# Performance work log

Measured on AMD Instinct MI355X. Metric: run time of the kernel, lower is better.

The kernel has to match this reference:

```python
import jax, jax.numpy as jnp
import numpy as np

T, B, V, E, H = 128, 32, 32000, 512, 1024
PAD = 0

def setup_inputs() -> dict:
    key = jax.random.key(0)
    ks = jax.random.split(key, 10)
    indices = jax.random.randint(ks[0], (T, B), 0, V)
    emb = jax.random.normal(ks[1], (V, E), jnp.float32) * 0.02
    s = 1.0 / np.sqrt(H).astype(np.float32)
    W_ih = jax.random.normal(ks[2], (4 * H, E), jnp.float32) * s
    W_hh = jax.random.normal(ks[3], (4 * H, H), jnp.float32) * s
    b_ih = jax.random.normal(ks[4], (4 * H,), jnp.float32) * 0.01
    b_hh = jax.random.normal(ks[5], (4 * H,), jnp.float32) * 0.01
    W_out = jax.random.normal(ks[6], (V, H), jnp.float32) * s
    b_out = jnp.zeros((V,), jnp.float32)
    h0 = jax.random.uniform(ks[7], (B, H), jnp.float32, -0.1, 0.1)
    c0 = jax.random.uniform(ks[8], (B, H), jnp.float32, -0.1, 0.1)
    return dict(indices=indices, emb=emb, W_ih=W_ih, W_hh=W_hh,
                b_ih=b_ih, b_hh=b_hh, W_out=W_out, b_out=b_out, h0=h0, c0=c0)

def reference(indices, emb, W_ih, W_hh, b_ih, b_hh, W_out, b_out, h0, c0):
    # embed + relu for all timesteps at once (dropout_rate=0.0 -> identity)
    x_all = jax.nn.relu(emb[indices[:-1]])   # [T-1, B, E]
    targets = indices[1:]                    # [T-1, B]

    def step(carry, inp):
        h, c, loss = carry
        x, tgt = inp
        # torch LSTM gate order: i, f, g, o
        gates = x @ W_ih.T + b_ih + h @ W_hh.T + b_hh   # [B, 4H]
        i, f, g, o = jnp.split(gates, 4, axis=-1)
        c = jax.nn.sigmoid(f) * c + jax.nn.sigmoid(i) * jnp.tanh(g)
        h = jax.nn.sigmoid(o) * jnp.tanh(c)
        logp = jax.nn.log_softmax(h @ W_out.T + b_out, axis=-1)  # [B, V]
        nll = -jnp.take_along_axis(logp, tgt[:, None], axis=-1)[:, 0]
        # NLLLoss(reduction='sum', ignore_index=PAD)
        loss = loss + jnp.sum(jnp.where(tgt != PAD, nll, 0.0))
        return (h, c, loss), None

    (_, _, loss), _ = jax.lax.scan(step, (h0, c0, jnp.float32(0.0)), (x_all, targets))
    return loss
```

## Files before the change

kernel.cpp:

```cpp
#include <hip/hip_runtime.h>
#include <hip/hip_bf16.h>
#include <hip/hip_cooperative_groups.h>
#include <math.h>

namespace cg = cooperative_groups;

typedef __bf16 bf16_t;
typedef bf16_t bf16x8 __attribute__((ext_vector_type(8)));
typedef float f32x4 __attribute__((ext_vector_type(4)));
typedef unsigned u32x2 __attribute__((ext_vector_type(2)));

#define T_SEQ 128
#define NB 32
#define NV 32000
#define NE 512
#define NH 1024
#define G4 4096
#define MROWS 4064
#define MPAD 4096

#define NBLK 256

__device__ __forceinline__ void g2lds16(const bf16_t* g, bf16_t* l) {
  __builtin_amdgcn_global_load_lds((const __attribute__((address_space(1))) void*)g,
                                   (__attribute__((address_space(3))) void*)l, 16, 0, 0);
}

__device__ __forceinline__ unsigned short bf16bits(float x) {
  bf16_t b = (bf16_t)x;
  return __builtin_bit_cast(unsigned short, b);
}

__global__ void k_prep(const int* __restrict__ idx, const float* __restrict__ emb,
                       const float* __restrict__ W_ih, const float* __restrict__ W_hh,
                       const float* __restrict__ b_ih, const float* __restrict__ b_hh,
                       const float* __restrict__ W_out, const float* __restrict__ h0,
                       bf16_t* __restrict__ W_ih_bf, bf16_t* __restrict__ W_hh_bf,
                       bf16_t* __restrict__ W_out_bf, bf16_t* __restrict__ x_bf,
                       bf16_t* __restrict__ h_all, bf16_t* __restrict__ h0_bf,
                       float* __restrict__ bc, float* __restrict__ rowS,
                       int* __restrict__ tgt, unsigned* __restrict__ bar) {
  const long nW_ih = 4096L * 512;
  const long nW_hh = 4096L * 1024;
  const long nW_out = 32000L * 1024;
  const long nX = 4096L * 512;
  const long nH0 = 32L * 1024;
  const long nHpad = 32L * 1024;
  const long NTOTAL = nW_ih + nW_hh + nW_out + nX + nH0 + nHpad + 3 * 4096L + 1024;
  long stride = (long)gridDim.x * blockDim.x;
  for (long i = (long)blockIdx.x * blockDim.x + threadIdx.x; i < NTOTAL; i += stride) {
    long j = i;
    if (j < nW_ih) { W_ih_bf[j] = (bf16_t)W_ih[j]; continue; }
    j -= nW_ih;
    if (j < nW_hh) { W_hh_bf[j] = (bf16_t)W_hh[j]; continue; }
    j -= nW_hh;
    if (j < nW_out) { W_out_bf[j] = (bf16_t)W_out[j]; continue; }
    j -= nW_out;
    if (j < nX) {
      long m = j >> 9; int e = (int)(j & 511);
      float x = 0.f;
      if (m < MROWS) { x = emb[(long)idx[m] * NE + e]; x = x > 0.f ? x : 0.f; }
      x_bf[j] = (bf16_t)x; continue;
    }
    j -= nX;
    if (j < nH0) { h0_bf[j] = (bf16_t)h0[j]; continue; }
    j -= nH0;
    if (j < nHpad) { h_all[4161536L + j] = (bf16_t)0.f; continue; }
    j -= nHpad;
    if (j < 4096) { bc[j] = b_ih[j] + b_hh[j]; continue; }
    j -= 4096;
    if (j < 4096) { rowS[j] = 0.f; continue; }
    j -= 4096;
    if (j < 4096) { tgt[j] = (j < MROWS) ? idx[j + NB] : 0; continue; }
    j -= 4096;
    { bar[j] = 0u; continue; }
  }
}

__global__ __launch_bounds__(256) void k_gemm1(const bf16_t* __restrict__ A,
                                               const bf16_t* __restrict__ B,
                                               const float* __restrict__ bc,
                                               bf16_t* __restrict__ C) {
  const int K = 512;
  int tid = threadIdx.x, wid = tid >> 6, lane = tid & 63;
  int wm = wid & 1, wn = wid >> 1;
  int quad = lane >> 4, l15 = lane & 15;
  int mBase = blockIdx.x * 64, nBase = blockIdx.y * 128;

  const bf16x8* pa0 = (const bf16x8*)(A + (long)(mBase + wm * 32 + l15) * K + quad * 8);
  const bf16x8* pa1 = (const bf16x8*)(A + (long)(mBase + wm * 32 + 16 + l15) * K + quad * 8);
  const bf16x8* pb[4];
#pragma unroll
  for (int j = 0; j < 4; ++j)
    pb[j] = (const bf16x8*)(B + (long)(nBase + wn * 64 + j * 16 + l15) * K + quad * 8);

  f32x4 acc[2][4];
#pragma unroll
  for (int mi = 0; mi < 2; ++mi)
#pragma unroll
    for (int ni = 0; ni < 4; ++ni) acc[mi][ni] = (f32x4){0.f, 0.f, 0.f, 0.f};

  for (int kk = 0; kk < K / 32; ++kk) {
    bf16x8 a0 = pa0[kk * 4], a1 = pa1[kk * 4];
    bf16x8 b0 = pb[0][kk * 4], b1 = pb[1][kk * 4], b2 = pb[2][kk * 4], b3 = pb[3][kk * 4];
    acc[0][0] = __builtin_amdgcn_mfma_f32_16x16x32_bf16(a0, b0, acc[0][0], 0, 0, 0);
    acc[0][1] = __builtin_amdgcn_mfma_f32_16x16x32_bf16(a0, b1, acc[0][1], 0, 0, 0);
    acc[0][2] = __builtin_amdgcn_mfma_f32_16x16x32_bf16(a0, b2, acc[0][2], 0, 0, 0);
    acc[0][3] = __builtin_amdgcn_mfma_f32_16x16x32_bf16(a0, b3, acc[0][3], 0, 0, 0);
    acc[1][0] = __builtin_amdgcn_mfma_f32_16x16x32_bf16(a1, b0, acc[1][0], 0, 0, 0);
    acc[1][1] = __builtin_amdgcn_mfma_f32_16x16x32_bf16(a1, b1, acc[1][1], 0, 0, 0);
    acc[1][2] = __builtin_amdgcn_mfma_f32_16x16x32_bf16(a1, b2, acc[1][2], 0, 0, 0);
    acc[1][3] = __builtin_amdgcn_mfma_f32_16x16x32_bf16(a1, b3, acc[1][3], 0, 0, 0);
  }
#pragma unroll
  for (int ni = 0; ni < 4; ++ni) {
    int col = nBase + wn * 64 + ni * 16 + l15;
    float bcv = bc[col];
#pragma unroll
    for (int mi = 0; mi < 2; ++mi)
#pragma unroll
      for (int r = 0; r < 4; ++r) {
        int row = mBase + wm * 32 + mi * 16 + quad * 4 + r;
        C[(long)row * G4 + col] = (bf16_t)(acc[mi][ni][r] + bcv);
      }
  }
}

__global__ __launch_bounds__(512) void k_rec8(const bf16_t* __restrict__ gates_x,
                                              const bf16_t* __restrict__ W_hh_bf,
                                              const bf16_t* __restrict__ h0_bf,
                                              bf16_t* __restrict__ h_all,
                                              const float* __restrict__ c0,
                                              unsigned* __restrict__ bar) {
  __shared__ __align__(16) float red[32 * 68];

  int bid = blockIdx.x;
  int mi = bid & 1;
  int hb = bid >> 1;
  int gbase = hb * 8;
  int tid = threadIdx.x, wid = tid >> 6, lane = tid & 63;
  int cg = wid & 1, kh = wid >> 1;
  int quad = lane >> 4, l15 = lane & 15;

  unsigned* genp = bar + mi * 512 + 288;
  unsigned* flagp = bar + mi * 512 + 320 + hb;
  const unsigned* fp2 = bar + mi * 512 + 320 + (lane << 1);
  bool isagg = (bid < 2) && (wid == 7);

  int wrow = (cg ? 2048 : 0) + ((l15 & 8) ? 1024 : 0) + gbase + (l15 & 7);
  const bf16x8* pw = (const bf16x8*)(W_hh_bf + (long)wrow * NH + kh * 256 + quad * 8);
  bf16x8 wfrag[8];
#pragma unroll
  for (int kk = 0; kk < 8; ++kk) wfrag[kk] = pw[kk * 4];

  int pb = tid >> 2, pu2 = (tid & 3) * 2;
  int u0 = gbase + pu2;
  int bglob = mi * 16 + pb;
  float cst0 = 0.f, cst1 = 0.f;
  if (tid < 64) {
    cst0 = c0[(long)bglob * NH + u0];
    cst1 = c0[(long)bglob * NH + u0 + 1];
  }
  unsigned* h32 = (unsigned*)h_all;

  for (int t = 0; t < T_SEQ - 1; ++t) {
    unsigned gxi2 = 0, gxf2 = 0, gxg2 = 0, gxo2 = 0;
    if (tid < 64) {
      const unsigned* gp = (const unsigned*)(gates_x + (long)(t * NB + bglob) * G4);
      int q = u0 >> 1;
      gxi2 = gp[q]; gxf2 = gp[512 + q]; gxg2 = gp[1024 + q]; gxo2 = gp[1536 + q];
    }

    if (t > 0) {
      if (isagg) {
        unsigned need = (unsigned)t;
        while (1) {
          u32x2 fv;
          asm volatile("global_load_dwordx2 %0, %1, off sc0 sc1\n\t"
                       "s_waitcnt vmcnt(0)"
                       : "=&v"(fv) : "v"(fp2) : "memory");
          if (__all((fv.x >= need) & (fv.y >= need))) break;
          __builtin_amdgcn_s_sleep(1);
        }
        if (lane == 0)
          __hip_atomic_store(genp, (unsigned)t, __ATOMIC_RELAXED,
                             __HIP_MEMORY_SCOPE_AGENT);
      }
      if (tid == 0) {
        unsigned need = (unsigned)t;
        while (__hip_atomic_load(genp, __ATOMIC_RELAXED,
                                 __HIP_MEMORY_SCOPE_AGENT) < need)
          __builtin_amdgcn_s_sleep(1);
      }
    }
    __syncthreads();
    asm volatile("" ::: "memory");

    const bf16_t* hp = (t == 0) ? h0_bf : (h_all + (long)(t - 1) * NB * NH);
    const bf16x8* pa = (const bf16x8*)(hp + (long)(mi * 16 + l15) * NH + kh * 256 + quad * 8);
    f32x4 acc = (f32x4){0.f, 0.f, 0.f, 0.f};
#pragma unroll
    for (int kk = 0; kk < 8; ++kk) {
      bf16x8 a = pa[kk * 4];
      acc = __builtin_amdgcn_mfma_f32_16x16x32_bf16(a, wfrag[kk], acc, 0, 0, 0);
    }
#pragma unroll
    for (int r = 0; r < 4; ++r) {
      int row = (cg << 4) + (quad << 2) + r;
      red[row * 68 + (l15 << 2) + kh] = acc[r];
    }
    __syncthreads();

    if (tid < 64) {
      const float* rc = red;
      float hv[2];
#pragma unroll
      for (int d = 0; d < 2; ++d) {
        int q = pu2 + d;
        float4 vi = *(const float4*)(rc + pb * 68 + (q << 2));
        float4 vf = *(const float4*)(rc + pb * 68 + ((8 + q) << 2));
        float4 vg = *(const float4*)(rc + (16 + pb) * 68 + (q << 2));
        float4 vo = *(const float4*)(rc + (16 + pb) * 68 + ((8 + q) << 2));
        unsigned bi = d ? (gxi2 & 0xffff0000u) : (gxi2 << 16);
        unsigned bff = d ? (gxf2 & 0xffff0000u) : (gxf2 << 16);
        unsigned bg = d ? (gxg2 & 0xffff0000u) : (gxg2 << 16);
        unsigned bo = d ? (gxo2 & 0xffff0000u) : (gxo2 << 16);
        float iv = vi.x + vi.y + vi.z + vi.w + __builtin_bit_cast(float, bi);
        float fv = vf.x + vf.y + vf.z + vf.w + __builtin_bit_cast(float, bff);
        float gv = vg.x + vg.y + vg.z + vg.w + __builtin_bit_cast(float, bg);
        float ov = vo.x + vo.y + vo.z + vo.w + __builtin_bit_cast(float, bo);
        float si = 1.f / (1.f + __expf(-iv));
        float sf = 1.f / (1.f + __expf(-fv));
        float so = 1.f / (1.f + __expf(-ov));
        float tg = 1.f - 2.f / (__expf(2.f * gv) + 1.f);
        float& cs = d ? cst1 : cst0;
        cs = sf * cs + si * tg;
        float th = 1.f - 2.f / (__expf(2.f * cs) + 1.f);
        hv[d] = so * th;
      }
      unsigned pack = (unsigned)bf16bits(hv[0]) | ((unsigned)bf16bits(hv[1]) << 16);
      __hip_atomic_store(&h32[(long)(t * NB + bglob) * 512 + (u0 >> 1)], pack,
                         __ATOMIC_RELAXED, __HIP_MEMORY_SCOPE_AGENT);
      if (t < T_SEQ - 2) {
        asm volatile("" ::: "memory");
        if (tid == 0) {
          __builtin_amdgcn_s_waitcnt(0x0f70);
          asm volatile("" ::: "memory");
          __hip_atomic_store(flagp, (unsigned)(t + 1), __ATOMIC_RELAXED,
                             __HIP_MEMORY_SCOPE_AGENT);
        }
      }
    }
  }
}

__global__ __launch_bounds__(256) void k_gemm2(const bf16_t* __restrict__ A,
                                               const bf16_t* __restrict__ B,
                                               const float* __restrict__ b_out,
                                               float* __restrict__ rowS) {
  __shared__ bf16_t As[128 * 32];
  __shared__ bf16_t Bs[128 * 32];
  const int K = 1024;
  int tid = threadIdx.x, wid = tid >> 6, lane = tid & 63;
  int wm = wid & 1, wn = wid >> 1;
  int quad = lane >> 4, l15 = lane & 15;
  int mBase = blockIdx.x * 128, nBase = blockIdx.y * 128;

  int rc = lane >> 2, seg = lane & 3;
  int cA0 = 2 * wid, cA1 = 2 * wid + 1;
  const bf16_t* gA0 = A + (size_t)(mBase + cA0 * 16 + rc) * K + seg * 8;
  const bf16_t* gA1 = A + (size_t)(mBase + cA1 * 16 + rc) * K + seg * 8;
  const bf16_t* gB0 = B + (size_t)(nBase + cA0 * 16 + rc) * K + seg * 8;
  const bf16_t* gB1 = B + (size_t)(nBase + cA1 * 16 + rc) * K + seg * 8;
  bf16_t* lA0 = As + cA0 * 512;
  bf16_t* lA1 = As + cA1 * 512;
  bf16_t* lB0 = Bs + cA0 * 512;
  bf16_t* lB1 = Bs + cA1 * 512;

  const bf16x8* pa[4];
  const bf16x8* pbf[4];
#pragma unroll
  for (int i = 0; i < 4; ++i) {
    pa[i] = (const bf16x8*)(As + (wm * 64 + i * 16 + l15) * 32 + quad * 8);
    pbf[i] = (const bf16x8*)(Bs + (wn * 64 + i * 16 + l15) * 32 + quad * 8);
  }

  f32x4 acc[4][4];
#pragma unroll
  for (int i = 0; i < 4; ++i)
#pragma unroll
    for (int j = 0; j < 4; ++j) acc[i][j] = (f32x4){0.f, 0.f, 0.f, 0.f};

  for (int kt = 0; kt < K / 32; ++kt) {
    g2lds16(gA0 + kt * 32, lA0);
    g2lds16(gA1 + kt * 32, lA1);
    g2lds16(gB0 + kt * 32, lB0);
    g2lds16(gB1 + kt * 32, lB1);
    __syncthreads();

    bf16x8 af[4], bf[4];
#pragma unroll
    for (int i = 0; i < 4; ++i) { af[i] = *pa[i]; bf[i] = *pbf[i]; }
#pragma unroll
    for (int i = 0; i < 4; ++i)
#pragma unroll
      for (int j = 0; j < 4; ++j)
        acc[i][j] = __builtin_amdgcn_mfma_f32_16x16x32_bf16(af[i], bf[j], acc[i][j], 0, 0, 0);
    __syncthreads();
  }

#pragma unroll
  for (int i = 0; i < 4; ++i) {
    float rs[4] = {0.f, 0.f, 0.f, 0.f};
#pragma unroll
    for (int j = 0; j < 4; ++j) {
      int col = nBase + wn * 64 + j * 16 + l15;
      float bb = b_out[col];
#pragma unroll
      for (int r = 0; r < 4; ++r) rs[r] += __expf(acc[i][j][r] + bb);
    }
#pragma unroll
    for (int r = 0; r < 4; ++r) {
#pragma unroll
      for (int s = 1; s < 16; s <<= 1) rs[r] += __shfl_xor(rs[r], s);
      if (l15 == 0) {
        int row = mBase + wm * 64 + i * 16 + quad * 4 + r;
        if (row < MROWS) atomicAdd(&rowS[row], rs[r]);
      }
    }
  }
}

__global__ __launch_bounds__(256) void k_tgt(const bf16_t* __restrict__ h_all,
                                             const bf16_t* __restrict__ W_out_bf,
                                             const float* __restrict__ b_out,
                                             const int* __restrict__ tgt,
                                             float* __restrict__ tgt_logit) {
  int gw = (int)((blockIdx.x * blockDim.x + threadIdx.x) >> 6);
  int lane = threadIdx.x & 63;
  if (gw >= MROWS) return;
  int v = tgt[gw];
  const bf16x8* ph = (const bf16x8*)(h_all + (long)gw * NH + lane * 16);
  const bf16x8* pw = (const bf16x8*)(W_out_bf + (long)v * NH + lane * 16);
  float acc = 0.f;
#pragma unroll
  for (int j = 0; j < 2; ++j) {
    bf16x8 h8 = ph[j], w8 = pw[j];
#pragma unroll
    for (int q = 0; q < 8; ++q) acc += (float)h8[q] * (float)w8[q];
  }
#pragma unroll
  for (int s = 1; s < 64; s <<= 1) acc += __shfl_xor(acc, s);
  if (lane == 0) tgt_logit[gw] = acc + b_out[v];
}

__global__ __launch_bounds__(256) void k_loss(const float* __restrict__ rowS,
                                              const float* __restrict__ tl,
                                              const int* __restrict__ tgt,
                                              float* __restrict__ out) {
  __shared__ float sm[256];
  float s = 0.f;
  for (int i = threadIdx.x; i < MROWS; i += 256)
    if (tgt[i] != 0) s += logf(rowS[i]) - tl[i];
  sm[threadIdx.x] = s;
  __syncthreads();
  for (int off = 128; off > 0; off >>= 1) {
    if (threadIdx.x < off) sm[threadIdx.x] += sm[threadIdx.x + off];
    __syncthreads();
  }
  if (threadIdx.x == 0) out[0] = sm[0];
}

extern "C" void kernel_launch(void* const* d_in, const int* in_sizes, int n_in,
                              void* d_out, int out_size, void* d_ws, size_t ws_size,
                              hipStream_t stream) {
  const int* idx = (const int*)d_in[0];
  const float* emb = (const float*)d_in[1];
  const float* W_ih = (const float*)d_in[2];
  const float* W_hh = (const float*)d_in[3];
  const float* b_ih = (const float*)d_in[4];
  const float* b_hh = (const float*)d_in[5];
  const float* W_out = (const float*)d_in[6];
  const float* b_out = (const float*)d_in[7];
  const float* h0 = (const float*)d_in[8];
  const float* c0 = (const float*)d_in[9];

  char* ws = (char*)d_ws;
  bf16_t* W_ih_bf = (bf16_t*)ws;            ws += 4096L * 512 * 2;
  bf16_t* W_hh_bf = (bf16_t*)ws;            ws += 4096L * 1024 * 2;
  bf16_t* W_out_bf = (bf16_t*)ws;           ws += 32000L * 1024 * 2;
  bf16_t* x_bf = (bf16_t*)ws;               ws += 4096L * 512 * 2;
  bf16_t* gates_x = (bf16_t*)ws;            ws += 4096L * 4096 * 2;
  bf16_t* h_all = (bf16_t*)ws;              ws += 4096L * 1024 * 2;
  bf16_t* h0_bf = (bf16_t*)ws;              ws += 32L * 1024 * 2;
  float* bc = (float*)ws;                   ws += 4096L * 4;
  float* rowS = (float*)ws;                 ws += 4096L * 4;
  float* tgt_logit = (float*)ws;            ws += 4096L * 4;
  int* tgt = (int*)ws;                      ws += 4096L * 4;
  unsigned* bar = (unsigned*)ws;            ws += 1024L * 4;

  k_prep<<<4096, 256, 0, stream>>>(idx, emb, W_ih, W_hh, b_ih, b_hh, W_out, h0,
                                   W_ih_bf, W_hh_bf, W_out_bf, x_bf, h_all, h0_bf,
                                   bc, rowS, tgt, bar);

  k_gemm1<<<dim3(64, 32), 256, 0, stream>>>(x_bf, W_ih_bf, bc, gates_x);

  {
    void* args[] = {(void*)&gates_x, (void*)&W_hh_bf, (void*)&h0_bf, (void*)&h_all,
                    (void*)&c0, (void*)&bar};
    hipLaunchCooperativeKernel((void*)k_rec8, dim3(NBLK), dim3(512), args, 0, stream);
  }

  k_gemm2<<<dim3(32, 250), 256, 0, stream>>>(h_all, W_out_bf, b_out, rowS);

  k_tgt<<<1016, 256, 0, stream>>>(h_all, W_out_bf, b_out, tgt, tgt_logit);

  k_loss<<<1, 256, 0, stream>>>(rowS, tgt_logit, tgt, (float*)d_out);
}
```

Measured before the change: 1.332 ms.

## Use sentinel-filled hidden state to replace store-wait before flag in recurrence

The prep kernel now converts weights and embeddings four elements at a time with vectorized loads and stores, and fills the h_all buffer with a 0xFFFFFFFF sentinel. The recurrent kernel drops the s_waitcnt that made the flag store wait for the h stores to complete. Instead, readers check each loaded h fragment for the sentinel and re-poll with cache-bypassing loads until real data arrives. This takes the store-drain latency off the per-step critical path, at the cost of extra compare work and possible spin reloads, and it relies on no valid bf16 pair ever matching the sentinel pattern.

```diff
diff --git a/kernel.cpp b/kernel.cpp
--- a/kernel.cpp
+++ b/kernel.cpp
@@ -9,6 +9,7 @@
 typedef bf16_t bf16x8 __attribute__((ext_vector_type(8)));
 typedef float f32x4 __attribute__((ext_vector_type(4)));
 typedef unsigned u32x2 __attribute__((ext_vector_type(2)));
+typedef unsigned u32x4 __attribute__((ext_vector_type(4)));
 
 #define T_SEQ 128
 #define NB 32
@@ -20,6 +21,7 @@
 #define MPAD 4096
 
 #define NBLK 256
+#define SENT 0xFFFFFFFFu
 
 __device__ __forceinline__ void g2lds16(const bf16_t* g, bf16_t* l) {
   __builtin_amdgcn_global_load_lds((const __attribute__((address_space(1))) void*)g,
@@ -29,6 +31,15 @@
 __device__ __forceinline__ unsigned short bf16bits(float x) {
   bf16_t b = (bf16_t)x;
   return __builtin_bit_cast(unsigned short, b);
+}
+
+__device__ __forceinline__ void cvt4(const float* __restrict__ s,
+                                     bf16_t* __restrict__ d, long j) {
+  float4 v = *(const float4*)(s + j * 4);
+  uint2 o;
+  o.x = (unsigned)bf16bits(v.x) | ((unsigned)bf16bits(v.y) << 16);
+  o.y = (unsigned)bf16bits(v.z) | ((unsigned)bf16bits(v.w) << 16);
+  *(uint2*)(d + j * 4) = o;
 }
 
 __global__ void k_prep(const int* __restrict__ idx, const float* __restrict__ emb,
@@ -40,33 +51,47 @@
                        bf16_t* __restrict__ h_all, bf16_t* __restrict__ h0_bf,
                        float* __restrict__ bc, float* __restrict__ rowS,
                        int* __restrict__ tgt, unsigned* __restrict__ bar) {
-  const long nW_ih = 4096L * 512;
-  const long nW_hh = 4096L * 1024;
-  const long nW_out = 32000L * 1024;
-  const long nX = 4096L * 512;
-  const long nH0 = 32L * 1024;
-  const long nHpad = 32L * 1024;
-  const long NTOTAL = nW_ih + nW_hh + nW_out + nX + nH0 + nHpad + 3 * 4096L + 1024;
+  const long n4_Wih = 4096L * 512 / 4;
+  const long n4_Whh = 4096L * 1024 / 4;
+  const long n4_Wout = 32000L * 1024 / 4;
+  const long n4_X = 4096L * 512 / 4;
+  const long n4_H0 = 32L * 1024 / 4;
+  const long n4_Hall = 4096L * 1024 / 8;
+  const long nSentinel = 4064L * 128;
+  const long nScal = 3 * 4096L + 1024;
+  const long NTOT = n4_Wih + n4_Whh + n4_Wout + n4_X + n4_H0 + n4_Hall + nScal;
   long stride = (long)gridDim.x * blockDim.x;
-  for (long i = (long)blockIdx.x * blockDim.x + threadIdx.x; i < NTOTAL; i += stride) {
+  for (long i = (long)blockIdx.x * blockDim.x + threadIdx.x; i < NTOT; i += stride) {
     long j = i;
-    if (j < nW_ih) { W_ih_bf[j] = (bf16_t)W_ih[j]; continue; }
-    j -= nW_ih;
-    if (j < nW_hh) { W_hh_bf[j] = (bf16_t)W_hh[j]; continue; }
-    j -= nW_hh;
-    if (j < nW_out) { W_out_bf[j] = (bf16_t)W_out[j]; continue; }
-    j -= nW_out;
-    if (j < nX) {
-      long m = j >> 9; int e = (int)(j & 511);
-      float x = 0.f;
-      if (m < MROWS) { x = emb[(long)idx[m] * NE + e]; x = x > 0.f ? x : 0.f; }
-      x_bf[j] = (bf16_t)x; continue;
-    }
-    j -= nX;
-    if (j < nH0) { h0_bf[j] = (bf16_t)h0[j]; continue; }
-    j -= nH0;
-    if (j < nHpad) { h_all[4161536L + j] = (bf16_t)0.f; continue; }
-    j -= nHpad;
+    if (j < n4_Wih) { cvt4(W_ih, W_ih_bf, j); continue; }
+    j -= n4_Wih;
+    if (j < n4_Whh) { cvt4(W_hh, W_hh_bf, j); continue; }
+    j -= n4_Whh;
+    if (j < n4_Wout) { cvt4(W_out, W_out_bf, j); continue; }
+    j -= n4_Wout;
+    if (j < n4_X) {
+      long m = j >> 7; int e4 = (int)(j & 127);
+      uint2 o; o.x = 0u; o.y = 0u;
+      if (m < MROWS) {
+        float4 v = *(const float4*)(emb + (long)idx[m] * NE + e4 * 4);
+        v.x = fmaxf(v.x, 0.f); v.y = fmaxf(v.y, 0.f);
+        v.z = fmaxf(v.z, 0.f); v.w = fmaxf(v.w, 0.f);
+        o.x = (unsigned)bf16bits(v.x) | ((unsigned)bf16bits(v.y) << 16);
+        o.y = (unsigned)bf16bits(v.z) | ((unsigned)bf16bits(v.w) << 16);
+      }
+      *(uint2*)(x_bf + m * 512 + e4 * 4) = o;
+      continue;
+    }
+    j -= n4_X;
+    if (j < n4_H0) { cvt4(h0, h0_bf, j); continue; }
+    j -= n4_H0;
+    if (j < n4_Hall) {
+      unsigned v = (j < nSentinel) ? SENT : 0u;
+      uint4 s; s.x = v; s.y = v; s.z = v; s.w = v;
+      ((uint4*)h_all)[j] = s;
+      continue;
+    }
+    j -= n4_Hall;
     if (j < 4096) { bc[j] = b_ih[j] + b_hh[j]; continue; }
     j -= 4096;
     if (j < 4096) { rowS[j] = 0.f; continue; }
@@ -126,7 +151,7 @@
   }
 }
 
-__global__ __launch_bounds__(512) void k_rec8(const bf16_t* __restrict__ gates_x,
+__global__ __launch_bounds__(512) void k_rec9(const bf16_t* __restrict__ gates_x,
                                               const bf16_t* __restrict__ W_hh_bf,
                                               const bf16_t* __restrict__ h0_bf,
                                               bf16_t* __restrict__ h_all,
@@ -196,14 +221,47 @@
     __syncthreads();
     asm volatile("" ::: "memory");
 
-    const bf16_t* hp = (t == 0) ? h0_bf : (h_all + (long)(t - 1) * NB * NH);
-    const bf16x8* pa = (const bf16x8*)(hp + (long)(mi * 16 + l15) * NH + kh * 256 + quad * 8);
+    bf16x8 hfr[8];
+    if (t == 0) {
+      const bf16x8* pa0 =
+          (const bf16x8*)(h0_bf + (long)(mi * 16 + l15) * NH + kh * 256 + quad * 8);
+#pragma unroll
+      for (int kk = 0; kk < 8; ++kk) hfr[kk] = pa0[kk * 4];
+    } else {
+      const bf16_t* hb8 = h_all + (long)(t - 1) * NB * NH +
+                          (long)(mi * 16 + l15) * NH + kh * 256 + quad * 8;
+      const bf16x8* pa = (const bf16x8*)hb8;
+#pragma unroll
+      for (int kk = 0; kk < 8; ++kk) hfr[kk] = pa[kk * 4];
+      unsigned bad = 0;
+#pragma unroll
+      for (int kk = 0; kk < 8; ++kk) {
+        u32x4 w = __builtin_bit_cast(u32x4, hfr[kk]);
+        bad |= (unsigned)(w.x == SENT) | (unsigned)(w.y == SENT) |
+               (unsigned)(w.z == SENT) | (unsigned)(w.w == SENT);
+      }
+      while (!__all(bad == 0)) {
+        __builtin_amdgcn_s_sleep(1);
+        u32x4 hw[8];
+#pragma unroll
+        for (int kk = 0; kk < 8; ++kk)
+          asm volatile("global_load_dwordx4 %0, %1, off sc0 sc1"
+                       : "=&v"(hw[kk]) : "v"(hb8 + kk * 32) : "memory");
+        asm volatile("s_waitcnt vmcnt(0)" ::: "memory");
+        bad = 0;
+#pragma unroll
+        for (int kk = 0; kk < 8; ++kk) {
+          bad |= (unsigned)(hw[kk].x == SENT) | (unsigned)(hw[kk].y == SENT) |
+                 (unsigned)(hw[kk].z == SENT) | (unsigned)(hw[kk].w == SENT);
+          hfr[kk] = __builtin_bit_cast(bf16x8, hw[kk]);
+        }
+      }
+    }
+
     f32x4 acc = (f32x4){0.f, 0.f, 0.f, 0.f};
 #pragma unroll
-    for (int kk = 0; kk < 8; ++kk) {
-      bf16x8 a = pa[kk * 4];
-      acc = __builtin_amdgcn_mfma_f32_16x16x32_bf16(a, wfrag[kk], acc, 0, 0, 0);
-    }
+    for (int kk = 0; kk < 8; ++kk)
+      acc = __builtin_amdgcn_mfma_f32_16x16x32_bf16(hfr[kk], wfrag[kk], acc, 0, 0, 0);
 #pragma unroll
     for (int r = 0; r < 4; ++r) {
       int row = (cg << 4) + (quad << 2) + r;
@@ -241,15 +299,9 @@
       unsigned pack = (unsigned)bf16bits(hv[0]) | ((unsigned)bf16bits(hv[1]) << 16);
       __hip_atomic_store(&h32[(long)(t * NB + bglob) * 512 + (u0 >> 1)], pack,
                          __ATOMIC_RELAXED, __HIP_MEMORY_SCOPE_AGENT);
-      if (t < T_SEQ - 2) {
-        asm volatile("" ::: "memory");
-        if (tid == 0) {
-          __builtin_amdgcn_s_waitcnt(0x0f70);
-          asm volatile("" ::: "memory");
-          __hip_atomic_store(flagp, (unsigned)(t + 1), __ATOMIC_RELAXED,
-                             __HIP_MEMORY_SCOPE_AGENT);
-        }
-      }
+      if (t < T_SEQ - 2 && tid == 0)
+        __hip_atomic_store(flagp, (unsigned)(t + 1), __ATOMIC_RELAXED,
+                           __HIP_MEMORY_SCOPE_AGENT);
     }
   }
 }
@@ -408,7 +460,7 @@
   {
     void* args[] = {(void*)&gates_x, (void*)&W_hh_bf, (void*)&h0_bf, (void*)&h_all,
                     (void*)&c0, (void*)&bar};
-    hipLaunchCooperativeKernel((void*)k_rec8, dim3(NBLK), dim3(512), args, 0, stream);
+    hipLaunchCooperativeKernel((void*)k_rec9, dim3(NBLK), dim3(512), args, 0, stream);
   }
 
   k_gemm2<<<dim3(32, 250), 256, 0, stream>>>(h_all, W_out_bf, b_out, rowS);
```

After: 1.261 ms. -5.3%, faster.
